# Kernel tuning notes

Measured on AMD Instinct MI355X. Metric: run time of the kernel, lower is better.

The kernel has to match this reference:

```python
import jax, jax.numpy as jnp
import numpy as np

V, E, H = 32000, 512, 1024  # vocab, embed_dim, hidden_dim
N, T = 32, 256              # batch, seq_len


def setup_inputs() -> dict:
    key = jax.random.key(0)
    ks = jax.random.split(key, 8)
    s = 1.0 / np.sqrt(H)
    return {
        "words": jax.random.randint(ks[0], (N, T), 0, V),
        "hidden_state": jnp.zeros((N, H), jnp.float32),
        "embed_w": jax.random.uniform(ks[1], (V, E), minval=-1.0, maxval=1.0) * 0.1,
        "w_ih": jax.random.uniform(ks[2], (3 * H, E), minval=-s, maxval=s),
        "w_hh": jax.random.uniform(ks[3], (3 * H, H), minval=-s, maxval=s),
        "b_ih": jax.random.uniform(ks[4], (3 * H,), minval=-s, maxval=s),
        "b_hh": jax.random.uniform(ks[5], (3 * H,), minval=-s, maxval=s),
        "emit_w": jax.random.uniform(ks[6], (V, H), minval=-s, maxval=s),
        "emit_b": jnp.zeros((V,), jnp.float32),
    }


def reference(words, hidden_state, embed_w, w_ih, w_hh, b_ih, b_hh, emit_w, emit_b):
    n = words.shape[0]
    emb = embed_w[words]                      # [N, T, E]
    xs = (jnp.swapaxes(emb[:, :-1], 0, 1),    # [T-1, N, E] inputs x_{t-1}
          jnp.swapaxes(words[:, 1:], 0, 1))   # [T-1, N]    targets w_t

    def gru_cell(x, h):
        gi = x @ w_ih.T + b_ih                # [N, 3H]
        gh = h @ w_hh.T + b_hh                # [N, 3H]
        i_r, i_z, i_n = jnp.split(gi, 3, axis=-1)
        h_r, h_z, h_n = jnp.split(gh, 3, axis=-1)
        r = jax.nn.sigmoid(i_r + h_r)
        z = jax.nn.sigmoid(i_z + h_z)
        nn_ = jnp.tanh(i_n + r * h_n)
        return (1.0 - z) * nn_ + z * h

    def step(carry, inp):
        h, acc = carry
        x, w = inp
        h = gru_cell(x, h)
        logits = h @ emit_w.T + emit_b        # [N, V]
        logp = jax.nn.log_softmax(logits, axis=-1)
        ll = jnp.take_along_axis(logp, w[:, None], axis=1)[:, 0]  # [N]
        return (h, acc + ll), None

    acc0 = jnp.zeros((n,), hidden_state.dtype)
    (h_final, word_marginals), _ = jax.lax.scan(step, (hidden_state, acc0), xs)
    return word_marginals, h_final
```

## Files before the change

kernel.cpp:

```cpp
#include <hip/hip_runtime.h>
#include <cstdint>

#define V_    32000
#define E_    512
#define H_    1024
#define N_    32
#define T_    256
#define TS    255
#define NWG_B 64
#define CB_   250
#define RB_   64
#define MROW  8192
#define GI_CB 24

typedef _Float16 f16;
typedef _Float16 half8 __attribute__((ext_vector_type(8)));
typedef float floatx4 __attribute__((ext_vector_type(4)));
typedef unsigned long long u64;


__global__ void prep_emit16(const float* __restrict__ emit_w, f16* __restrict__ out) {
  const int64_t nchunk = (int64_t)V_ * H_ / 8;
  int64_t i = (int64_t)blockIdx.x * blockDim.x + threadIdx.x;
  for (; i < nchunk; i += (int64_t)gridDim.x * blockDim.x) {
    const float4* src = (const float4*)(emit_w + i * 8);
    float4 a = src[0], b = src[1];
    half8 h;
    h[0] = (f16)a.x; h[1] = (f16)a.y; h[2] = (f16)a.z; h[3] = (f16)a.w;
    h[4] = (f16)b.x; h[5] = (f16)b.y; h[6] = (f16)b.z; h[7] = (f16)b.w;
    *(half8*)(out + i * 8) = h;
  }
}

__global__ void prep_whh(const float* __restrict__ w_hh, f16* __restrict__ whh) {
  int idx = blockIdx.x * blockDim.x + threadIdx.x;
  if (idx >= 192 * 32 * 64) return;
  int lane = idx & 63;
  int kt   = (idx >> 6) & 31;
  int jt   = (idx >> 6) >> 5;
  int col  = jt * 16 + (lane & 15);
  int k0   = kt * 32 + (lane >> 4) * 8;
  const float* src = w_hh + (int64_t)col * H_ + k0;
  half8 h;
#pragma unroll
  for (int i = 0; i < 8; ++i) h[i] = (f16)src[i];
  *(half8*)(whh + (int64_t)idx * 8) = h;
}

__global__ void prep_wih16(const float* __restrict__ w_ih, f16* __restrict__ out) {
  int idx = blockIdx.x * blockDim.x + threadIdx.x;
  if (idx >= 3072 * 512 / 8) return;
  const float4* src = (const float4*)(w_ih + (int64_t)idx * 8);
  float4 a = src[0], b = src[1];
  half8 h;
  h[0] = (f16)a.x; h[1] = (f16)a.y; h[2] = (f16)a.z; h[3] = (f16)a.w;
  h[4] = (f16)b.x; h[5] = (f16)b.y; h[6] = (f16)b.z; h[7] = (f16)b.w;
  *(half8*)(out + (int64_t)idx * 8) = h;
}

__global__ void prep_xemb(const int* __restrict__ words, const float* __restrict__ embed_w,
                          f16* __restrict__ xemb) {
  int idx = blockIdx.x * blockDim.x + threadIdx.x;
  if (idx >= TS * N_ * (E_ / 8)) return;
  int u = idx & 63;
  int n = (idx >> 6) & 31;
  int t = idx >> 11;
  int word = words[n * T_ + t];
  const float* src = embed_w + (int64_t)word * E_ + u * 8;
  half8 h;
#pragma unroll
  for (int i = 0; i < 8; ++i) h[i] = (f16)src[i];
  *(half8*)(xemb + (int64_t)(t * N_ + n) * E_ + u * 8) = h;
}

__global__ void prep_init(const float* __restrict__ h0, f16* __restrict__ xh,
                          unsigned* __restrict__ slots) {
  int idx = blockIdx.x * blockDim.x + threadIdx.x;
  if (idx < N_ * H_) {
    f16 v = (f16)h0[idx];
    xh[idx] = v;
    xh[N_ * H_ + idx] = v;
  }
  if (idx < 512 * 16) slots[idx] = 0;
}


#define LDK 72

__launch_bounds__(256, 2)
__global__ void gi_gemm(const f16* __restrict__ xemb, const f16* __restrict__ wih16,
                        f16* __restrict__ gi2) {
  const int cb = blockIdx.x % GI_CB;
  const int rb = blockIdx.x / GI_CB;
  const int tid = threadIdx.x;
  const int w = tid >> 6, lane = tid & 63;
  const int wm = w & 1, wn = w >> 1;
  const int l15 = lane & 15, l4 = lane >> 4;

  __shared__ f16 lA[128 * LDK];
  __shared__ f16 lB[128 * LDK];

  floatx4 acc[4][4];
#pragma unroll
  for (int mt = 0; mt < 4; ++mt)
#pragma unroll
    for (int nt = 0; nt < 4; ++nt) { acc[mt][nt][0] = 0.f; acc[mt][nt][1] = 0.f; acc[mt][nt][2] = 0.f; acc[mt][nt][3] = 0.f; }

  const f16* gA = xemb + (int64_t)rb * 128 * E_;
  const f16* gB = wih16 + (int64_t)cb * 128 * E_;

  for (int kb = 0; kb < 8; ++kb) {
    __syncthreads();
#pragma unroll
    for (int i = 0; i < 4; ++i) {
      int idx = i * 256 + tid;
      int row = idx >> 3, u = idx & 7;
      int64_t goff = (int64_t)row * E_ + kb * 64 + u * 8;
      *(half8*)(lA + row * LDK + u * 8) = *(const half8*)(gA + goff);
      *(half8*)(lB + row * LDK + u * 8) = *(const half8*)(gB + goff);
    }
    __syncthreads();
#pragma unroll
    for (int ks = 0; ks < 2; ++ks) {
      half8 af[4], bf[4];
#pragma unroll
      for (int mt = 0; mt < 4; ++mt)
        af[mt] = *(const half8*)(lA + (wm * 64 + mt * 16 + l15) * LDK + ks * 32 + l4 * 8);
#pragma unroll
      for (int nt = 0; nt < 4; ++nt)
        bf[nt] = *(const half8*)(lB + (wn * 64 + nt * 16 + l15) * LDK + ks * 32 + l4 * 8);
#pragma unroll
      for (int mt = 0; mt < 4; ++mt)
#pragma unroll
        for (int nt = 0; nt < 4; ++nt)
          acc[mt][nt] = __builtin_amdgcn_mfma_f32_16x16x32_f16(af[mt], bf[nt], acc[mt][nt], 0, 0, 0);
    }
  }

#pragma unroll
  for (int mt = 0; mt < 4; ++mt) {
#pragma unroll
    for (int r = 0; r < 4; ++r) {
      int g = rb * 128 + wm * 64 + mt * 16 + l4 * 4 + r;
      if (g < TS * N_) {
        int tt = g >> 5, n = g & 31;
        f16* gb = gi2 + ((int64_t)tt * 3072 + cb * 128 + wn * 64) * 32 + n;
#pragma unroll
        for (int nt = 0; nt < 4; ++nt)
          gb[(nt * 16 + l15) * 32] = (f16)acc[mt][nt][r];
      }
    }
  }
}


__device__ inline u64 aload64(const void* p) {
  return __hip_atomic_load((const u64*)p, __ATOMIC_RELAXED, __HIP_MEMORY_SCOPE_AGENT);
}
__device__ inline unsigned aload32(const void* p) {
  return __hip_atomic_load((const unsigned*)p, __ATOMIC_RELAXED, __HIP_MEMORY_SCOPE_AGENT);
}

__launch_bounds__(512, 1)
__global__ void phaseB(const f16* __restrict__ whh, const f16* __restrict__ gi2,
                       f16* __restrict__ xh, const float* __restrict__ b_ih,
                       const float* __restrict__ b_hh, f16* __restrict__ hall,
                       float* __restrict__ out, unsigned* __restrict__ slots) {
  const int b = blockIdx.x;
  const int tid = threadIdx.x;
  const int w = tid >> 6;
  const int lane = tid & 63;
  const int l15 = lane & 15, l4 = lane >> 4;

  __shared__ float part[2][8][32][49];

  const int n_g = tid & 31;
  const int jl = tid >> 5;
  const int j = b * 16 + jl;
  const float biasr = b_ih[j] + b_hh[j];
  const float biasz = b_ih[H_ + j] + b_hh[H_ + j];
  const float bihn = b_ih[2 * H_ + j];
  const float bhhn = b_hh[2 * H_ + j];

  half8 wf[3][4];
#pragma unroll
  for (int g = 0; g < 3; ++g) {
    int jt = g * 64 + b;
#pragma unroll
    for (int k = 0; k < 4; ++k)
      wf[g][k] = *(const half8*)(whh + (((int64_t)jt * 32 + (w * 4 + k)) * 64 + lane) * 8);
  }

  const unsigned* myflag = slots + ((unsigned)(8 * w + (lane >> 3)) * 8 + (lane & 7)) * 16;
  unsigned* ownflag = slots + ((unsigned)b * 8 + w) * 16;

  float hold = (float)xh[n_g * H_ + j];

  for (int t = 0; t < TS; ++t) {
    const f16* xh_rd = xh + (t & 1) * (N_ * H_);
    f16* xh_wr = xh + ((t + 1) & 1) * (N_ * H_);

    const f16* gbase = gi2 + (int64_t)t * 3072 * 32 + n_g;
    float gvr = (float)gbase[(int64_t)j * 32];
    float gvz = (float)gbase[(int64_t)(H_ + j) * 32];
    float gvn = (float)gbase[(int64_t)(2 * H_ + j) * 32];

    while (aload32(myflag) < (unsigned)t) __builtin_amdgcn_s_sleep(1);

    half8 a0[4], a1[4];
#pragma unroll
    for (int k = 0; k < 4; ++k) {
      const f16* base = xh_rd + (w * 4 + k) * 32 + l4 * 8;
      union { half8 h; u64 u[2]; } x0, x1;
      const u64* p0 = (const u64*)(base + (int64_t)l15 * H_);
      const u64* p1 = (const u64*)(base + (int64_t)(l15 + 16) * H_);
      x0.u[0] = aload64(p0); x0.u[1] = aload64(p0 + 1);
      x1.u[0] = aload64(p1); x1.u[1] = aload64(p1 + 1);
      a0[k] = x0.h; a1[k] = x1.h;
    }

    floatx4 acc[3][2];
#pragma unroll
    for (int g = 0; g < 3; ++g)
#pragma unroll
      for (int m = 0; m < 2; ++m) { acc[g][m][0] = 0.f; acc[g][m][1] = 0.f; acc[g][m][2] = 0.f; acc[g][m][3] = 0.f; }

#pragma unroll
    for (int k = 0; k < 4; ++k) {
#pragma unroll
      for (int g = 0; g < 3; ++g) {
        acc[g][0] = __builtin_amdgcn_mfma_f32_16x16x32_f16(a0[k], wf[g][k], acc[g][0], 0, 0, 0);
        acc[g][1] = __builtin_amdgcn_mfma_f32_16x16x32_f16(a1[k], wf[g][k], acc[g][1], 0, 0, 0);
      }
    }

    float (*pp)[32][49] = part[t & 1];
#pragma unroll
    for (int g = 0; g < 3; ++g)
#pragma unroll
      for (int m = 0; m < 2; ++m)
#pragma unroll
        for (int r = 0; r < 4; ++r)
          pp[w][m * 16 + l4 * 4 + r][g * 16 + l15] = acc[g][m][r];
    __syncthreads();

    float gr = biasr + gvr, gz = biasz + gvz, gin = bihn + gvn, ghn = bhhn;
#pragma unroll
    for (int ww = 0; ww < 8; ++ww) {
      gr += pp[ww][n_g][jl];
      gz += pp[ww][n_g][16 + jl];
      ghn += pp[ww][n_g][32 + jl];
    }
    float rg = 1.f / (1.f + __expf(-gr));
    float zg = 1.f / (1.f + __expf(-gz));
    float nn = tanhf(gin + rg * ghn);
    float hnew = (1.f - zg) * nn + zg * hold;

    unsigned short hb = __builtin_bit_cast(unsigned short, (f16)hnew);
    unsigned other = (unsigned)__shfl_xor((int)(unsigned)hb, 32, 64);
    unsigned packed = (unsigned)hb | (other << 16);
    if (!(jl & 1)) {
      __hip_atomic_store((unsigned*)(xh_wr + n_g * H_ + j), packed,
                         __ATOMIC_RELAXED, __HIP_MEMORY_SCOPE_AGENT);
    }
    if (t < TS - 1) {
      __builtin_amdgcn_s_waitcnt(0);
      if (lane == 0)
        __hip_atomic_store(ownflag, (unsigned)(t + 1),
                           __ATOMIC_RELAXED, __HIP_MEMORY_SCOPE_AGENT);
    }
    if (!(jl & 1))
      *(unsigned*)(hall + ((int64_t)t * N_ + n_g) * H_ + j) = packed;
    if (t == TS - 1) out[32 + n_g * H_ + j] = hnew;

    hold = (float)(f16)hnew;
  }
}


__device__ inline void gload_lds16(const f16* g, f16* l) {
  __builtin_amdgcn_global_load_lds((const __attribute__((address_space(1))) void*)g,
                                   (__attribute__((address_space(3))) void*)l, 16, 0, 0);
}

__launch_bounds__(256, 2)
__global__ void phaseC(const f16* __restrict__ hall, const f16* __restrict__ emit16,
                       const float* __restrict__ emit_b, float* __restrict__ spart) {
  const int wgid = (blockIdx.x & 7) * 2000 + (blockIdx.x >> 3);
  const int cb = wgid >> 6;
  const int rb = wgid & 63;
  const int tid = threadIdx.x;
  const int w = tid >> 6, lane = tid & 63;
  const int wm = w & 1, wn = w >> 1;
  const int l15 = lane & 15, l4 = lane >> 4;

  __shared__ f16 lA[128 * 64];
  __shared__ f16 lB[128 * 64];
  __shared__ float rs[2][128];

  floatx4 acc[4][4];
#pragma unroll
  for (int mt = 0; mt < 4; ++mt)
#pragma unroll
    for (int nt = 0; nt < 4; ++nt) { acc[mt][nt][0] = 0.f; acc[mt][nt][1] = 0.f; acc[mt][nt][2] = 0.f; acc[mt][nt][3] = 0.f; }

  const f16* gA = hall + (int64_t)rb * 128 * H_;
  const f16* gB = emit16 + (int64_t)cb * 128 * H_;

  const int lrow8 = lane >> 3;
  const int sc = (lane & 7) ^ lrow8;
  const int rdx = (l15 & 7) << 3;

  for (int kb = 0; kb < 16; ++kb) {
    __syncthreads();
#pragma unroll
    for (int i = 0; i < 4; ++i) {
      const int r0 = w * 32 + i * 8;
      const int64_t goff = (int64_t)(r0 + lrow8) * H_ + kb * 64 + sc * 8;
      gload_lds16(gA + goff, lA + r0 * 64);
      gload_lds16(gB + goff, lB + r0 * 64);
    }
    __syncthreads();
#pragma unroll
    for (int ks = 0; ks < 2; ++ks) {
      half8 af[4], bf[4];
      const int col = (ks * 32 + l4 * 8) ^ rdx;
#pragma unroll
      for (int mt = 0; mt < 4; ++mt)
        af[mt] = *(const half8*)(lA + (wm * 64 + mt * 16 + l15) * 64 + col);
#pragma unroll
      for (int nt = 0; nt < 4; ++nt)
        bf[nt] = *(const half8*)(lB + (wn * 64 + nt * 16 + l15) * 64 + col);
#pragma unroll
      for (int mt = 0; mt < 4; ++mt)
#pragma unroll
        for (int nt = 0; nt < 4; ++nt)
          acc[mt][nt] = __builtin_amdgcn_mfma_f32_16x16x32_f16(af[mt], bf[nt], acc[mt][nt], 0, 0, 0);
    }
  }

  float eb[4];
#pragma unroll
  for (int nt = 0; nt < 4; ++nt) eb[nt] = emit_b[cb * 128 + wn * 64 + nt * 16 + l15];

#pragma unroll
  for (int mt = 0; mt < 4; ++mt) {
#pragma unroll
    for (int r = 0; r < 4; ++r) {
      float s = 0.f;
#pragma unroll
      for (int nt = 0; nt < 4; ++nt) s += __expf(acc[mt][nt][r] + eb[nt]);
#pragma unroll
      for (int off = 1; off < 16; off <<= 1) s += __shfl_xor(s, off, 64);
      if (l15 == 0) rs[wn][wm * 64 + mt * 16 + l4 * 4 + r] = s;
    }
  }
  __syncthreads();
  if (tid < 128)
    spart[(int64_t)cb * MROW + rb * 128 + tid] = rs[0][tid] + rs[1][tid];
}


__global__ void target_dots(const f16* __restrict__ hall, const f16* __restrict__ emit16,
                            const int* __restrict__ words, const float* __restrict__ emit_b,
                            float* __restrict__ tlog) {
  int r = blockIdx.x * 4 + (threadIdx.x >> 6);
  if (r >= TS * N_) return;
  int lane = threadIdx.x & 63;
  int t = r >> 5, n = r & 31;
  int tgt = words[n * T_ + t + 1];
  const f16* ha = hall + (int64_t)r * H_;
  const f16* ebp = emit16 + (int64_t)tgt * H_;
  float s = 0.f;
#pragma unroll
  for (int c = 0; c < 2; ++c) {
    int k = c * 512 + lane * 8;
    half8 a = *(const half8*)(ha + k);
    half8 b = *(const half8*)(ebp + k);
#pragma unroll
    for (int i = 0; i < 8; ++i) s += (float)a[i] * (float)b[i];
  }
#pragma unroll
  for (int off = 1; off < 64; off <<= 1) s += __shfl_xor(s, off, 64);
  if (lane == 0) tlog[r] = s + emit_b[tgt];
}

__global__ void reduce_lse(const float* __restrict__ spart, const float* __restrict__ tlog,
                           float* __restrict__ lval) {
  int r = blockIdx.x * blockDim.x + threadIdx.x;
  if (r >= TS * N_) return;
  float s = 0.f;
  for (int cb = 0; cb < CB_; ++cb) s += spart[(int64_t)cb * MROW + r];
  lval[r] = tlog[r] - logf(s);
}

__global__ void finalize(const float* __restrict__ lval, float* __restrict__ out) {
  __shared__ float ps[8][32];
  int n = threadIdx.x & 31, sl = threadIdx.x >> 5;
  float s = 0.f;
  for (int i = 0; i < 32; ++i) {
    int t = sl * 32 + i;
    if (t < TS) s += lval[t * N_ + n];
  }
  ps[sl][n] = s;
  __syncthreads();
  if (threadIdx.x < 32) {
    float tot = 0.f;
#pragma unroll
    for (int k = 0; k < 8; ++k) tot += ps[k][threadIdx.x];
    out[threadIdx.x] = tot;
  }
}


extern "C" void kernel_launch(void* const* d_in, const int* in_sizes, int n_in,
                              void* d_out, int out_size, void* d_ws, size_t ws_size,
                              hipStream_t stream) {
  (void)in_sizes; (void)n_in; (void)out_size; (void)ws_size;
  const int*   words   = (const int*)d_in[0];
  const float* h0      = (const float*)d_in[1];
  const float* embed_w = (const float*)d_in[2];
  const float* w_ih    = (const float*)d_in[3];
  const float* w_hh    = (const float*)d_in[4];
  const float* b_ih    = (const float*)d_in[5];
  const float* b_hh    = (const float*)d_in[6];
  const float* emit_w  = (const float*)d_in[7];
  const float* emit_b  = (const float*)d_in[8];
  float* out = (float*)d_out;

  char* ws = (char*)d_ws;
  f16*      big    = (f16*)(ws + 0);
  f16*      gi2    = big;
  f16*      emit16 = big;
  f16*      whh    = (f16*)(ws + 65536000);
  f16*      wih16  = (f16*)(ws + 71827456);
  float*    spart  = (float*)(ws + 71827456);
  f16*      xemb   = (f16*)(ws + 74973184);
  f16*      xh     = (f16*)(ws + 83361792);
  f16*      hall   = (f16*)(ws + 83492864);
  float*    tlog   = (float*)(ws + 100270080);
  float*    lval   = (float*)(ws + 100302720);
  unsigned* slots  = (unsigned*)(ws + 100335360);

  hipLaunchKernelGGL(prep_whh, dim3(1536), dim3(256), 0, stream, w_hh, whh);
  hipLaunchKernelGGL(prep_wih16, dim3(768), dim3(256), 0, stream, w_ih, wih16);
  hipLaunchKernelGGL(prep_xemb, dim3(2040), dim3(256), 0, stream, words, embed_w, xemb);
  hipLaunchKernelGGL(prep_init, dim3(128), dim3(256), 0, stream, h0, xh, slots);
  hipLaunchKernelGGL(gi_gemm, dim3(RB_ * GI_CB), dim3(256), 0, stream, xemb, wih16, gi2);
  hipLaunchKernelGGL(phaseB, dim3(NWG_B), dim3(512), 0, stream, whh, gi2, xh, b_ih, b_hh, hall, out, slots);
  hipLaunchKernelGGL(prep_emit16, dim3(4096), dim3(256), 0, stream, emit_w, emit16);
  hipLaunchKernelGGL(phaseC, dim3(RB_ * CB_), dim3(256), 0, stream, hall, emit16, emit_b, spart);
  hipLaunchKernelGGL(target_dots, dim3((TS * N_ + 3) / 4), dim3(256), 0, stream, hall, emit16, words, emit_b, tlog);
  hipLaunchKernelGGL(reduce_lse, dim3((TS * N_ + 255) / 256), dim3(256), 0, stream, spart, tlog, lval);
  hipLaunchKernelGGL(finalize, dim3(1), dim3(256), 0, stream, lval, out);
}
```

Baseline: 2.685 ms.

## Restructure GRU recurrence to one wave per workgroup with LDS-resident weights

The recurrent phase now runs one 64-lane wave per workgroup that covers the full K=1024 reduction. Its slice of W_hh is staged once into LDS, and the previous hidden state is read straight from the hall history buffer instead of a double-buffered xh scratch. This removes the per-step shared-memory partial-sum reduction, the __syncthreads barrier and the 8-way flag polling per wave; each lane now polls a single producer flag. In exchange, each step runs a long serial chain of 192 MFMAs and 64 global loads in one wave. The hidden-state reads are also plain loads rather than atomic loads, which leans on cache coherence across CUs.

```diff
diff --git a/kernel.cpp b/kernel.cpp
--- a/kernel.cpp
+++ b/kernel.cpp
@@ -76,12 +76,8 @@
 __global__ void prep_init(const float* __restrict__ h0, f16* __restrict__ xh,
                           unsigned* __restrict__ slots) {
   int idx = blockIdx.x * blockDim.x + threadIdx.x;
-  if (idx < N_ * H_) {
-    f16 v = (f16)h0[idx];
-    xh[idx] = v;
-    xh[N_ * H_ + idx] = v;
-  }
-  if (idx < 512 * 16) slots[idx] = 0;
+  if (idx < N_ * H_) xh[idx] = (f16)h0[idx];
+  if (idx < 1024) slots[idx] = 0;
 }
 
 
@@ -154,70 +150,58 @@
 }
 
 
-__device__ inline u64 aload64(const void* p) {
-  return __hip_atomic_load((const u64*)p, __ATOMIC_RELAXED, __HIP_MEMORY_SCOPE_AGENT);
-}
 __device__ inline unsigned aload32(const void* p) {
   return __hip_atomic_load((const unsigned*)p, __ATOMIC_RELAXED, __HIP_MEMORY_SCOPE_AGENT);
 }
 
-__launch_bounds__(512, 1)
+__launch_bounds__(64, 1)
 __global__ void phaseB(const f16* __restrict__ whh, const f16* __restrict__ gi2,
-                       f16* __restrict__ xh, const float* __restrict__ b_ih,
+                       const f16* __restrict__ h0f16, const float* __restrict__ b_ih,
                        const float* __restrict__ b_hh, f16* __restrict__ hall,
                        float* __restrict__ out, unsigned* __restrict__ slots) {
   const int b = blockIdx.x;
-  const int tid = threadIdx.x;
-  const int w = tid >> 6;
-  const int lane = tid & 63;
+  const int lane = threadIdx.x;
   const int l15 = lane & 15, l4 = lane >> 4;
-
-  __shared__ float part[2][8][32][49];
-
-  const int n_g = tid & 31;
-  const int jl = tid >> 5;
-  const int j = b * 16 + jl;
+  const int j = b * 16 + l15;
+
+  __shared__ half8 lw[3 * 32 * 64];
+
+  for (int i = 0; i < 96; ++i) {
+    int e = i * 64 + lane;
+    int g  = e >> 11;
+    int kt = (e >> 6) & 31;
+    int le = e & 63;
+    lw[e] = *(const half8*)(whh + (((int64_t)(g * 64 + b) * 32 + kt) * 64 + le) * 8);
+  }
+  __syncthreads();
+
   const float biasr = b_ih[j] + b_hh[j];
   const float biasz = b_ih[H_ + j] + b_hh[H_ + j];
-  const float bihn = b_ih[2 * H_ + j];
-  const float bhhn = b_hh[2 * H_ + j];
-
-  half8 wf[3][4];
-#pragma unroll
-  for (int g = 0; g < 3; ++g) {
-    int jt = g * 64 + b;
-#pragma unroll
-    for (int k = 0; k < 4; ++k)
-      wf[g][k] = *(const half8*)(whh + (((int64_t)jt * 32 + (w * 4 + k)) * 64 + lane) * 8);
-  }
-
-  const unsigned* myflag = slots + ((unsigned)(8 * w + (lane >> 3)) * 8 + (lane & 7)) * 16;
-  unsigned* ownflag = slots + ((unsigned)b * 8 + w) * 16;
-
-  float hold = (float)xh[n_g * H_ + j];
+  const float bihn  = b_ih[2 * H_ + j];
+  const float bhhn  = b_hh[2 * H_ + j];
+
+  float hold[2][4];
+#pragma unroll
+  for (int m = 0; m < 2; ++m)
+#pragma unroll
+    for (int r = 0; r < 4; ++r)
+      hold[m][r] = (float)h0f16[(m * 16 + l4 * 4 + r) * H_ + j];
+
+  const unsigned* pollp = slots + lane * 16;
+  unsigned* ownflag = slots + b * 16;
 
   for (int t = 0; t < TS; ++t) {
-    const f16* xh_rd = xh + (t & 1) * (N_ * H_);
-    f16* xh_wr = xh + ((t + 1) & 1) * (N_ * H_);
-
-    const f16* gbase = gi2 + (int64_t)t * 3072 * 32 + n_g;
-    float gvr = (float)gbase[(int64_t)j * 32];
-    float gvz = (float)gbase[(int64_t)(H_ + j) * 32];
-    float gvn = (float)gbase[(int64_t)(2 * H_ + j) * 32];
-
-    while (aload32(myflag) < (unsigned)t) __builtin_amdgcn_s_sleep(1);
-
-    half8 a0[4], a1[4];
-#pragma unroll
-    for (int k = 0; k < 4; ++k) {
-      const f16* base = xh_rd + (w * 4 + k) * 32 + l4 * 8;
-      union { half8 h; u64 u[2]; } x0, x1;
-      const u64* p0 = (const u64*)(base + (int64_t)l15 * H_);
-      const u64* p1 = (const u64*)(base + (int64_t)(l15 + 16) * H_);
-      x0.u[0] = aload64(p0); x0.u[1] = aload64(p0 + 1);
-      x1.u[0] = aload64(p1); x1.u[1] = aload64(p1 + 1);
-      a0[k] = x0.h; a1[k] = x1.h;
-    }
+    const f16* gp = gi2 + ((int64_t)t * 3072 + j) * 32 + l4 * 4;
+    u64 gvu[3][2];
+#pragma unroll
+    for (int g = 0; g < 3; ++g)
+#pragma unroll
+      for (int m = 0; m < 2; ++m)
+        gvu[g][m] = *(const u64*)(gp + g * (H_ * 32) + m * 16);
+
+    while (aload32(pollp) < (unsigned)t) __builtin_amdgcn_s_sleep(1);
+
+    const f16* hp = (t == 0) ? h0f16 : (hall + (int64_t)(t - 1) * N_ * H_);
 
     floatx4 acc[3][2];
 #pragma unroll
@@ -226,54 +210,66 @@
       for (int m = 0; m < 2; ++m) { acc[g][m][0] = 0.f; acc[g][m][1] = 0.f; acc[g][m][2] = 0.f; acc[g][m][3] = 0.f; }
 
 #pragma unroll
-    for (int k = 0; k < 4; ++k) {
+    for (int kt = 0; kt < 32; ++kt) {
+      const f16* base = hp + kt * 32 + l4 * 8;
+      half8 a0 = *(const half8*)(base + (int64_t)l15 * H_);
+      half8 a1 = *(const half8*)(base + (int64_t)(l15 + 16) * H_);
 #pragma unroll
       for (int g = 0; g < 3; ++g) {
-        acc[g][0] = __builtin_amdgcn_mfma_f32_16x16x32_f16(a0[k], wf[g][k], acc[g][0], 0, 0, 0);
-        acc[g][1] = __builtin_amdgcn_mfma_f32_16x16x32_f16(a1[k], wf[g][k], acc[g][1], 0, 0, 0);
+        half8 bf = lw[(g * 32 + kt) * 64 + lane];
+        acc[g][0] = __builtin_amdgcn_mfma_f32_16x16x32_f16(a0, bf, acc[g][0], 0, 0, 0);
+        acc[g][1] = __builtin_amdgcn_mfma_f32_16x16x32_f16(a1, bf, acc[g][1], 0, 0, 0);
       }
     }
 
-    float (*pp)[32][49] = part[t & 1];
-#pragma unroll
-    for (int g = 0; g < 3; ++g)
+    unsigned pk[2][4];
+    float hn[2][4];
+#pragma unroll
+    for (int m = 0; m < 2; ++m) {
+#pragma unroll
+      for (int r = 0; r < 4; ++r) {
+        float gvr = (float)__builtin_bit_cast(f16, (unsigned short)(gvu[0][m] >> (16 * r)));
+        float gvz = (float)__builtin_bit_cast(f16, (unsigned short)(gvu[1][m] >> (16 * r)));
+        float gvn = (float)__builtin_bit_cast(f16, (unsigned short)(gvu[2][m] >> (16 * r)));
+        float gr = biasr + gvr + acc[0][m][r];
+        float gz = biasz + gvz + acc[1][m][r];
+        float rg = 1.f / (1.f + __expf(-gr));
+        float zg = 1.f / (1.f + __expf(-gz));
+        float nn = tanhf(bihn + gvn + rg * (bhhn + acc[2][m][r]));
+        float hnew = (1.f - zg) * nn + zg * hold[m][r];
+        unsigned short hb = __builtin_bit_cast(unsigned short, (f16)hnew);
+        unsigned other = (unsigned)__shfl_xor((int)(unsigned)hb, 1, 64) & 0xffffu;
+        pk[m][r] = (unsigned)hb | (other << 16);
+        hn[m][r] = hnew;
+        hold[m][r] = (float)(f16)hnew;
+      }
+    }
+
+    f16* hw = hall + (int64_t)t * N_ * H_;
+    if (!(l15 & 1)) {
 #pragma unroll
       for (int m = 0; m < 2; ++m)
 #pragma unroll
-        for (int r = 0; r < 4; ++r)
-          pp[w][m * 16 + l4 * 4 + r][g * 16 + l15] = acc[g][m][r];
-    __syncthreads();
-
-    float gr = biasr + gvr, gz = biasz + gvz, gin = bihn + gvn, ghn = bhhn;
-#pragma unroll
-    for (int ww = 0; ww < 8; ++ww) {
-      gr += pp[ww][n_g][jl];
-      gz += pp[ww][n_g][16 + jl];
-      ghn += pp[ww][n_g][32 + jl];
-    }
-    float rg = 1.f / (1.f + __expf(-gr));
-    float zg = 1.f / (1.f + __expf(-gz));
-    float nn = tanhf(gin + rg * ghn);
-    float hnew = (1.f - zg) * nn + zg * hold;
-
-    unsigned short hb = __builtin_bit_cast(unsigned short, (f16)hnew);
-    unsigned other = (unsigned)__shfl_xor((int)(unsigned)hb, 32, 64);
-    unsigned packed = (unsigned)hb | (other << 16);
-    if (!(jl & 1)) {
-      __hip_atomic_store((unsigned*)(xh_wr + n_g * H_ + j), packed,
-                         __ATOMIC_RELAXED, __HIP_MEMORY_SCOPE_AGENT);
+        for (int r = 0; r < 4; ++r) {
+          int n = m * 16 + l4 * 4 + r;
+          __hip_atomic_store((unsigned*)(hw + n * H_ + j), pk[m][r],
+                             __ATOMIC_RELAXED, __HIP_MEMORY_SCOPE_AGENT);
+        }
     }
     if (t < TS - 1) {
       __builtin_amdgcn_s_waitcnt(0);
       if (lane == 0)
         __hip_atomic_store(ownflag, (unsigned)(t + 1),
                            __ATOMIC_RELAXED, __HIP_MEMORY_SCOPE_AGENT);
-    }
-    if (!(jl & 1))
-      *(unsigned*)(hall + ((int64_t)t * N_ + n_g) * H_ + j) = packed;
-    if (t == TS - 1) out[32 + n_g * H_ + j] = hnew;
-
-    hold = (float)(f16)hnew;
+    } else {
+#pragma unroll
+      for (int m = 0; m < 2; ++m)
+#pragma unroll
+        for (int r = 0; r < 4; ++r) {
+          int n = m * 16 + l4 * 4 + r;
+          out[32 + n * H_ + j] = hn[m][r];
+        }
+    }
   }
 }
 
@@ -447,7 +443,7 @@
   hipLaunchKernelGGL(prep_xemb, dim3(2040), dim3(256), 0, stream, words, embed_w, xemb);
   hipLaunchKernelGGL(prep_init, dim3(128), dim3(256), 0, stream, h0, xh, slots);
   hipLaunchKernelGGL(gi_gemm, dim3(RB_ * GI_CB), dim3(256), 0, stream, xemb, wih16, gi2);
-  hipLaunchKernelGGL(phaseB, dim3(NWG_B), dim3(512), 0, stream, whh, gi2, xh, b_ih, b_hh, hall, out, slots);
+  hipLaunchKernelGGL(phaseB, dim3(NWG_B), dim3(64), 0, stream, whh, gi2, xh, b_ih, b_hh, hall, out, slots);
   hipLaunchKernelGGL(prep_emit16, dim3(4096), dim3(256), 0, stream, emit_w, emit16);
   hipLaunchKernelGGL(phaseC, dim3(RB_ * CB_), dim3(256), 0, stream, hall, emit16, emit_b, spart);
   hipLaunchKernelGGL(target_dots, dim3((TS * N_ + 3) / 4), dim3(256), 0, stream, hall, emit16, words, emit_b, tlog);
```

New measurement: 3.155 ms. 17.5% more time.
